# Kernel tuning notes

Hardware: AMD Instinct MI355X
Metric: run time of the kernel (lower is better)

Reference implementation:

```python
import jax, jax.numpy as jnp
import numpy as np

LN_EPS = 1e-5
BN_EPS = 1e-5
HEADS = 8
KERNEL = 31
GROUP_SIZE = 8  # depthwise_conv groups = inner_dim // 8


def _ln(x, g, b):
    mu = jnp.mean(x, axis=-1, keepdims=True)
    var = jnp.var(x, axis=-1, keepdims=True)
    return (x - mu) * jax.lax.rsqrt(var + LN_EPS) * g + b


def _ff(x, g, b, w_in, b_in, w_out, b_out):
    h = _ln(x, g, b)
    y = h @ w_in.T + b_in
    a, c = jnp.split(y, 2, axis=-1)
    return (jax.nn.silu(a) * c) @ w_out.T + b_out


def _attn(x, g, b, wqkv, bqkv, wo, bo):
    B, S, _ = x.shape
    h = _ln(x, g, b)
    qkv = (h @ wqkv.T + bqkv).reshape(B, S, 3, HEADS, -1).transpose(2, 0, 3, 1, 4)
    q, k, v = qkv[0], qkv[1], qkv[2]  # [B,H,S,D]
    scale = q.shape[-1] ** -0.5
    scores = jnp.einsum('bhqd,bhkd->bhqk', q, k) * scale
    w = jax.nn.softmax(scores, axis=-1)
    o = jnp.einsum('bhqk,bhkd->bhqd', w, v)
    o = o.transpose(0, 2, 1, 3).reshape(B, S, -1)
    return o @ wo.T + bo


def _conv(x, g, b, pw1_w, pw1_b, dw_w, dw_b, bn_g, bn_b, bn_m, bn_v, pw2_w, pw2_b):
    h = _ln(x, g, b).transpose(0, 2, 1)  # [B, C, S]
    y = jnp.einsum('oc,bcs->bos', pw1_w[:, :, 0], h) + pw1_b[:, None]
    a, c = jnp.split(y, 2, axis=1)
    y = a * jax.nn.sigmoid(c)  # GLU over channel dim -> [B, inner, S]
    pad = (KERNEL - 1) // 2
    groups = y.shape[1] // dw_w.shape[1]  # inner_dim // 8
    y = jax.lax.conv_general_dilated(
        y, dw_w, window_strides=(1,), padding=[(pad, pad)],
        dimension_numbers=('NCH', 'OIH', 'NCH'), feature_group_count=groups)
    y = y + dw_b[:, None]
    y = (y - bn_m[:, None]) * jax.lax.rsqrt(bn_v[:, None] + BN_EPS) * bn_g[:, None] + bn_b[:, None]
    y = jax.nn.silu(y)
    y = jnp.einsum('oc,bcs->bos', pw2_w[:, :, 0], y) + pw2_b[:, None]
    return y.transpose(0, 2, 1)


def setup_inputs() -> dict:
    key = jax.random.key(0)
    dim, mult, exp = 512, 4, 2
    inner = dim * exp  # 1024
    ks = jax.random.split(key, 16)
    n = lambda k, shp: (jax.random.normal(k, shp, dtype=jnp.float32) * 0.02)
    d = {}
    d['x'] = jax.random.normal(ks[0], (8, 1024, dim), dtype=jnp.float32)
    # ff1
    d['ff1_g'] = jnp.ones((dim,), jnp.float32); d['ff1_b'] = jnp.zeros((dim,), jnp.float32)
    d['ff1_win'] = n(ks[1], (dim * mult * 2, dim)); d['ff1_bin'] = jnp.zeros((dim * mult * 2,), jnp.float32)
    d['ff1_wout'] = n(ks[2], (dim, dim * mult)); d['ff1_bout'] = jnp.zeros((dim,), jnp.float32)
    # attn
    d['attn_g'] = jnp.ones((dim,), jnp.float32); d['attn_b'] = jnp.zeros((dim,), jnp.float32)
    d['wqkv'] = n(ks[3], (3 * dim, dim)); d['bqkv'] = jnp.zeros((3 * dim,), jnp.float32)
    d['wo'] = n(ks[4], (dim, dim)); d['bo'] = jnp.zeros((dim,), jnp.float32)
    # conv
    d['conv_g'] = jnp.ones((dim,), jnp.float32); d['conv_b'] = jnp.zeros((dim,), jnp.float32)
    d['pw1_w'] = n(ks[5], (inner * 2, dim, 1)); d['pw1_b'] = jnp.zeros((inner * 2,), jnp.float32)
    d['dw_w'] = n(ks[6], (inner, GROUP_SIZE, KERNEL)); d['dw_b'] = jnp.zeros((inner,), jnp.float32)
    d['bn_g'] = jnp.ones((inner,), jnp.float32); d['bn_b'] = jnp.zeros((inner,), jnp.float32)
    d['bn_m'] = jnp.zeros((inner,), jnp.float32); d['bn_v'] = jnp.ones((inner,), jnp.float32)
    d['pw2_w'] = n(ks[7], (dim, inner, 1)); d['pw2_b'] = jnp.zeros((dim,), jnp.float32)
    # ff2
    d['ff2_g'] = jnp.ones((dim,), jnp.float32); d['ff2_b'] = jnp.zeros((dim,), jnp.float32)
    d['ff2_win'] = n(ks[8], (dim * mult * 2, dim)); d['ff2_bin'] = jnp.zeros((dim * mult * 2,), jnp.float32)
    d['ff2_wout'] = n(ks[9], (dim, dim * mult)); d['ff2_bout'] = jnp.zeros((dim,), jnp.float32)
    # final norm
    d['fn_g'] = jnp.ones((dim,), jnp.float32); d['fn_b'] = jnp.zeros((dim,), jnp.float32)
    return d


def reference(x, ff1_g, ff1_b, ff1_win, ff1_bin, ff1_wout, ff1_bout,
              attn_g, attn_b, wqkv, bqkv, wo, bo,
              conv_g, conv_b, pw1_w, pw1_b, dw_w, dw_b, bn_g, bn_b, bn_m, bn_v, pw2_w, pw2_b,
              ff2_g, ff2_b, ff2_win, ff2_bin, ff2_wout, ff2_bout, fn_g, fn_b):
    x = x + 0.5 * _ff(x, ff1_g, ff1_b, ff1_win, ff1_bin, ff1_wout, ff1_bout)
    x = x + _attn(x, attn_g, attn_b, wqkv, bqkv, wo, bo)
    x = x + _conv(x, conv_g, conv_b, pw1_w, pw1_b, dw_w, dw_b, bn_g, bn_b, bn_m, bn_v, pw2_w, pw2_b)
    x = x + 0.5 * _ff(x, ff2_g, ff2_b, ff2_win, ff2_bin, ff2_wout, ff2_bout)
    return _ln(x, fn_g, fn_b)
```

## Files before the change

kernel.cpp:

```cpp
#include <hip/hip_runtime.h>

#define SEQ   1024
#define BATCH 8
#define DIM   512
#define NTOK  (SEQ * BATCH)

typedef unsigned short ushort_t;
typedef unsigned int uint_t;
typedef __attribute__((ext_vector_type(8))) short s16x8;
typedef __attribute__((ext_vector_type(4))) float f32x4;

union F4 { float4 v; float f[4]; };

__device__ __forceinline__ float sigmoid_f(float x) { return 1.0f / (1.0f + expf(-x)); }
__device__ __forceinline__ float silu_f(float x)    { return x * sigmoid_f(x); }

__device__ __forceinline__ ushort_t f2bf(float x) {
  uint_t u = __float_as_uint(x);
  return (ushort_t)((u + 0x7FFFu + ((u >> 16) & 1u)) >> 16);
}
__device__ __forceinline__ float bf2f(ushort_t h) {
  return __uint_as_float(((uint_t)h) << 16);
}

__device__ __forceinline__ void gload16(const void* g, void* l) {
  __builtin_amdgcn_global_load_lds(
      (const __attribute__((address_space(1))) void*)g,
      (__attribute__((address_space(3))) void*)l,
      16, 0, 0);
}

struct CastArgs {
  const float* src[8];
  ushort_t*    dst[8];
  int          cum8[8];
};

__global__ __launch_bounds__(256) void f2b_multi(CastArgs a, int total8)
{
  const int i = blockIdx.x * 256 + threadIdx.x;
  if (i >= total8) return;
  int s = 0;
  #pragma unroll
  for (int k = 1; k < 8; ++k) s += (i >= a.cum8[k]) ? 1 : 0;
  const int j = i - a.cum8[s];
  const float* src = a.src[s] + (size_t)j * 8;
  F4 x0, x1;
  x0.v = *(const float4*)(src);
  x1.v = *(const float4*)(src + 4);
  uint4 o;
  o.x = (uint_t)f2bf(x0.f[0]) | ((uint_t)f2bf(x0.f[1]) << 16);
  o.y = (uint_t)f2bf(x0.f[2]) | ((uint_t)f2bf(x0.f[3]) << 16);
  o.z = (uint_t)f2bf(x1.f[0]) | ((uint_t)f2bf(x1.f[1]) << 16);
  o.w = (uint_t)f2bf(x1.f[2]) | ((uint_t)f2bf(x1.f[3]) << 16);
  *(uint4*)(a.dst[s] + (size_t)j * 8) = o;
}

template <int BF>
__global__ __launch_bounds__(256) void ln512_kernel(
    const float* __restrict__ in, const float* __restrict__ g,
    const float* __restrict__ b, void* __restrict__ outv)
{
  const int row = blockIdx.x * 4 + (threadIdx.x >> 6);
  const int l   = threadIdx.x & 63;
  const float* rp = in + (size_t)row * DIM + l * 8;
  F4 v0, v1;
  v0.v = *(const float4*)(rp);
  v1.v = *(const float4*)(rp + 4);
  float sum = 0.f, sq = 0.f;
  #pragma unroll
  for (int j = 0; j < 4; ++j) { sum += v0.f[j] + v1.f[j];
                                sq  += v0.f[j]*v0.f[j] + v1.f[j]*v1.f[j]; }
  #pragma unroll
  for (int m = 32; m >= 1; m >>= 1) {
    sum += __shfl_xor(sum, m, 64);
    sq  += __shfl_xor(sq,  m, 64);
  }
  const float mu   = sum * (1.0f / DIM);
  const float var  = sq * (1.0f / DIM) - mu * mu;
  const float rinv = rsqrtf(var + 1e-5f);
  F4 g0, g1, b0, b1;
  g0.v = *(const float4*)(g + l * 8);     g1.v = *(const float4*)(g + l * 8 + 4);
  b0.v = *(const float4*)(b + l * 8);     b1.v = *(const float4*)(b + l * 8 + 4);
  float o[8];
  #pragma unroll
  for (int j = 0; j < 4; ++j) {
    o[j]     = (v0.f[j] - mu) * rinv * g0.f[j] + b0.f[j];
    o[4 + j] = (v1.f[j] - mu) * rinv * g1.f[j] + b1.f[j];
  }
  if (BF) {
    uint4 u;
    u.x = (uint_t)f2bf(o[0]) | ((uint_t)f2bf(o[1]) << 16);
    u.y = (uint_t)f2bf(o[2]) | ((uint_t)f2bf(o[3]) << 16);
    u.z = (uint_t)f2bf(o[4]) | ((uint_t)f2bf(o[5]) << 16);
    u.w = (uint_t)f2bf(o[6]) | ((uint_t)f2bf(o[7]) << 16);
    *(uint4*)((ushort_t*)outv + (size_t)row * DIM + l * 8) = u;
  } else {
    F4 w0, w1;
    #pragma unroll
    for (int j = 0; j < 4; ++j) { w0.f[j] = o[j]; w1.f[j] = o[4 + j]; }
    *(float4*)((float*)outv + (size_t)row * DIM + l * 8)     = w0.v;
    *(float4*)((float*)outv + (size_t)row * DIM + l * 8 + 4) = w1.v;
  }
}

template <int EPI>
__global__ __launch_bounds__(256) void gemm_bf16(
    const ushort_t* __restrict__ A, const ushort_t* __restrict__ W,
    const float* __restrict__ bias, float* __restrict__ out,
    int N, int K, const float* __restrict__ res, float alpha)
{
  __shared__ ushort_t As[128 * 32];
  __shared__ ushort_t Ws[128 * 32];
  const int t    = threadIdx.x;
  const int lane = t & 63;
  const int w    = t >> 6;
  const int wm   = w >> 1, wn = w & 1;
  const int m0   = blockIdx.y << 7, n0 = blockIdx.x << 7;

  f32x4 acc[4][4] = {};

  const int lds0 = __builtin_amdgcn_readfirstlane((w * 64) * 16);
  const int lds1 = __builtin_amdgcn_readfirstlane((256 + w * 64) * 16);
  const int r0c  = t >> 2;
  const int r1c  = 64 + (t >> 2);
  const int cc   = (t & 3) << 3;

  for (int k0 = 0; k0 < K; k0 += 32) {
    gload16(A + (size_t)(m0 + r0c) * K + k0 + cc, (char*)As + lds0);
    gload16(A + (size_t)(m0 + r1c) * K + k0 + cc, (char*)As + lds1);
    gload16(W + (size_t)(n0 + r0c) * K + k0 + cc, (char*)Ws + lds0);
    gload16(W + (size_t)(n0 + r1c) * K + k0 + cc, (char*)Ws + lds1);
    __syncthreads();
    s16x8 a[4], b[4];
    #pragma unroll
    for (int i = 0; i < 4; ++i)
      a[i] = *(const s16x8*)&As[(wm * 64 + i * 16 + (lane & 15)) * 32 + ((lane >> 4) << 3)];
    #pragma unroll
    for (int j = 0; j < 4; ++j)
      b[j] = *(const s16x8*)&Ws[(wn * 64 + j * 16 + (lane & 15)) * 32 + ((lane >> 4) << 3)];
    #pragma unroll
    for (int i = 0; i < 4; ++i)
      #pragma unroll
      for (int j = 0; j < 4; ++j)
        acc[i][j] = __builtin_amdgcn_mfma_f32_16x16x32_bf16(a[i], b[j], acc[i][j], 0, 0, 0);
    __syncthreads();
  }

  #pragma unroll
  for (int i = 0; i < 4; ++i) {
    #pragma unroll
    for (int j = 0; j < 4; ++j) {
      const int col  = n0 + wn * 64 + j * 16 + (lane & 15);
      const int rowb = m0 + wm * 64 + i * 16 + ((lane >> 4) << 2);
      const float bc = bias[col];
      #pragma unroll
      for (int r = 0; r < 4; ++r) {
        const size_t idx = (size_t)(rowb + r) * N + col;
        float v = acc[i][j][r] + bc;
        if (EPI == 1) v = res[idx] + alpha * v;
        out[idx] = v;
      }
    }
  }
}

__global__ __launch_bounds__(256) void gemm_qkv_bf16(
    const ushort_t* __restrict__ A, const ushort_t* __restrict__ W,
    const float* __restrict__ bias, ushort_t* __restrict__ qkvb,
    ushort_t* __restrict__ Vt, int K)
{
  const int N = 1536;
  __shared__ ushort_t As[128 * 32];
  __shared__ ushort_t Ws[128 * 32];
  const int t    = threadIdx.x;
  const int lane = t & 63;
  const int w    = t >> 6;
  const int wm   = w >> 1, wn = w & 1;
  const int m0   = blockIdx.y << 7, n0 = blockIdx.x << 7;

  f32x4 acc[4][4] = {};

  const int lds0 = __builtin_amdgcn_readfirstlane((w * 64) * 16);
  const int lds1 = __builtin_amdgcn_readfirstlane((256 + w * 64) * 16);
  const int r0c  = t >> 2;
  const int r1c  = 64 + (t >> 2);
  const int cc   = (t & 3) << 3;

  for (int k0 = 0; k0 < K; k0 += 32) {
    gload16(A + (size_t)(m0 + r0c) * K + k0 + cc, (char*)As + lds0);
    gload16(A + (size_t)(m0 + r1c) * K + k0 + cc, (char*)As + lds1);
    gload16(W + (size_t)(n0 + r0c) * K + k0 + cc, (char*)Ws + lds0);
    gload16(W + (size_t)(n0 + r1c) * K + k0 + cc, (char*)Ws + lds1);
    __syncthreads();
    s16x8 a[4], b[4];
    #pragma unroll
    for (int i = 0; i < 4; ++i)
      a[i] = *(const s16x8*)&As[(wm * 64 + i * 16 + (lane & 15)) * 32 + ((lane >> 4) << 3)];
    #pragma unroll
    for (int j = 0; j < 4; ++j)
      b[j] = *(const s16x8*)&Ws[(wn * 64 + j * 16 + (lane & 15)) * 32 + ((lane >> 4) << 3)];
    #pragma unroll
    for (int i = 0; i < 4; ++i)
      #pragma unroll
      for (int j = 0; j < 4; ++j)
        acc[i][j] = __builtin_amdgcn_mfma_f32_16x16x32_bf16(a[i], b[j], acc[i][j], 0, 0, 0);
    __syncthreads();
  }

  #pragma unroll
  for (int i = 0; i < 4; ++i) {
    #pragma unroll
    for (int j = 0; j < 4; ++j) {
      const int col  = n0 + wn * 64 + j * 16 + (lane & 15);
      const int rowb = m0 + wm * 64 + i * 16 + ((lane >> 4) << 2);
      const float bc = bias[col];
      if (col < 1024) {
        #pragma unroll
        for (int r = 0; r < 4; ++r)
          qkvb[(size_t)(rowb + r) * N + col] = f2bf(acc[i][j][r] + bc);
      } else {
        const int vc = col - 1024;
        const int hh = vc >> 6, d = vc & 63;
        const int bb = rowb >> 10, s = rowb & 1023;
        ushort4 o;
        o.x = f2bf(acc[i][j][0] + bc);
        o.y = f2bf(acc[i][j][1] + bc);
        o.z = f2bf(acc[i][j][2] + bc);
        o.w = f2bf(acc[i][j][3] + bc);
        *(ushort4*)&Vt[(size_t)((bb * 8 + hh) * 64 + d) * 1024 + s] = o;
      }
    }
  }
}

template <int CGLU>
__global__ __launch_bounds__(256) void gemm_glu_bf16(
    const ushort_t* __restrict__ A, const ushort_t* __restrict__ W,
    const float* __restrict__ bias, ushort_t* __restrict__ out,
    int NG, int K)
{
  __shared__ ushort_t As[128 * 32];
  __shared__ ushort_t Was[64 * 32];
  __shared__ ushort_t Wcs[64 * 32];
  const int t    = threadIdx.x;
  const int lane = t & 63;
  const int w    = t >> 6;
  const int wm   = w >> 1, wn = w & 1;
  const int m0   = blockIdx.y << 7, n0 = blockIdx.x << 6;

  f32x4 acca[4][2] = {};
  f32x4 accc[4][2] = {};

  const int lds0 = __builtin_amdgcn_readfirstlane((w * 64) * 16);
  const int lds1 = __builtin_amdgcn_readfirstlane((256 + w * 64) * 16);
  const int r0c  = t >> 2;
  const int r1c  = 64 + (t >> 2);
  const int cc   = (t & 3) << 3;

  const ushort_t* Wc = W + (size_t)NG * K;

  for (int k0 = 0; k0 < K; k0 += 32) {
    gload16(A  + (size_t)(m0 + r0c) * K + k0 + cc, (char*)As  + lds0);
    gload16(A  + (size_t)(m0 + r1c) * K + k0 + cc, (char*)As  + lds1);
    gload16(W  + (size_t)(n0 + r0c) * K + k0 + cc, (char*)Was + lds0);
    gload16(Wc + (size_t)(n0 + r0c) * K + k0 + cc, (char*)Wcs + lds0);
    __syncthreads();
    s16x8 a[4], ba[2], bc[2];
    #pragma unroll
    for (int i = 0; i < 4; ++i)
      a[i] = *(const s16x8*)&As[(wm * 64 + i * 16 + (lane & 15)) * 32 + ((lane >> 4) << 3)];
    #pragma unroll
    for (int j = 0; j < 2; ++j) {
      const int roff = (wn * 32 + j * 16 + (lane & 15)) * 32 + ((lane >> 4) << 3);
      ba[j] = *(const s16x8*)&Was[roff];
      bc[j] = *(const s16x8*)&Wcs[roff];
    }
    #pragma unroll
    for (int i = 0; i < 4; ++i)
      #pragma unroll
      for (int j = 0; j < 2; ++j) {
        acca[i][j] = __builtin_amdgcn_mfma_f32_16x16x32_bf16(a[i], ba[j], acca[i][j], 0, 0, 0);
        accc[i][j] = __builtin_amdgcn_mfma_f32_16x16x32_bf16(a[i], bc[j], accc[i][j], 0, 0, 0);
      }
    __syncthreads();
  }

  #pragma unroll
  for (int i = 0; i < 4; ++i) {
    #pragma unroll
    for (int j = 0; j < 2; ++j) {
      const int col  = n0 + wn * 32 + j * 16 + (lane & 15);
      const int rowb = m0 + wm * 64 + i * 16 + ((lane >> 4) << 2);
      const float b1 = bias[col];
      const float b2 = bias[NG + col];
      #pragma unroll
      for (int r = 0; r < 4; ++r) {
        const float av = acca[i][j][r] + b1;
        const float cv = accc[i][j][r] + b2;
        const float o  = CGLU ? (av * sigmoid_f(cv)) : (silu_f(av) * cv);
        out[(size_t)(rowb + r) * NG + col] = f2bf(o);
      }
    }
  }
}

__global__ __launch_bounds__(256) void attn_mfma(
    const ushort_t* __restrict__ qkv, const ushort_t* __restrict__ Vt,
    ushort_t* __restrict__ out)
{
  __shared__ ushort_t Ks[64 * 64];
  __shared__ ushort_t Vs[64 * 64];
  __shared__ ushort_t Ps[4][16 * 64];

  const int t    = threadIdx.x;
  const int lane = t & 63;
  const int w    = t >> 6;
  const int i    = lane & 15;
  const int g    = lane >> 4;
  const int bh   = blockIdx.x;
  const int b    = bh >> 3, h = bh & 7;
  const int qt   = blockIdx.y;

  s16x8 qf[2];
  {
    const ushort_t* qrow = qkv + (size_t)(b * SEQ + qt * 64 + w * 16 + i) * 1536 + h * 64;
    qf[0] = *(const s16x8*)(qrow + g * 8);
    qf[1] = *(const s16x8*)(qrow + 32 + g * 8);
  }

  float m_[4], l_[4];
  f32x4 po[4] = {};
  #pragma unroll
  for (int r = 0; r < 4; ++r) { m_[r] = -1e30f; l_[r] = 0.0f; }

  const int e0   = w * 2;
  const int off0 = __builtin_amdgcn_readfirstlane(e0 * 1024);
  const int off1 = __builtin_amdgcn_readfirstlane(e0 * 1024 + 1024);

  for (int kvt = 0; kvt < 16; ++kvt) {
    __syncthreads();
    {
      const int s_a = e0 * 64 + lane;
      const int ra = s_a >> 3, ca = (s_a & 7) ^ (ra & 7);
      const int s_b = s_a + 64;
      const int rb = s_b >> 3, cb2 = (s_b & 7) ^ (rb & 7);
      gload16(qkv + (size_t)(b * SEQ + kvt * 64 + ra) * 1536 + 512 + h * 64 + ca * 8,
              (char*)Ks + off0);
      gload16(qkv + (size_t)(b * SEQ + kvt * 64 + rb) * 1536 + 512 + h * 64 + cb2 * 8,
              (char*)Ks + off1);
      gload16(Vt + (size_t)(bh * 64 + ra) * SEQ + kvt * 64 + ca * 8,
              (char*)Vs + off0);
      gload16(Vt + (size_t)(bh * 64 + rb) * SEQ + kvt * 64 + cb2 * 8,
              (char*)Vs + off1);
    }
    __syncthreads();

    f32x4 sc[4] = {};
    #pragma unroll
    for (int jj = 0; jj < 4; ++jj) {
      const int row = jj * 16 + i;
      #pragma unroll
      for (int dd = 0; dd < 2; ++dd) {
        const int byteoff = row * 128 + ((dd * 64 + g * 16) ^ ((row & 7) << 4));
        const s16x8 kf = *(const s16x8*)((const char*)Ks + byteoff);
        sc[jj] = __builtin_amdgcn_mfma_f32_16x16x32_bf16(qf[dd], kf, sc[jj], 0, 0, 0);
      }
    }

    #pragma unroll
    for (int r = 0; r < 4; ++r) {
      float v0 = sc[0][r] * 0.125f, v1 = sc[1][r] * 0.125f;
      float v2 = sc[2][r] * 0.125f, v3 = sc[3][r] * 0.125f;
      float mx = fmaxf(fmaxf(v0, v1), fmaxf(v2, v3));
      mx = fmaxf(mx, __shfl_xor(mx, 1));
      mx = fmaxf(mx, __shfl_xor(mx, 2));
      mx = fmaxf(mx, __shfl_xor(mx, 4));
      mx = fmaxf(mx, __shfl_xor(mx, 8));
      const float mn = fmaxf(m_[r], mx);
      const float al = __expf(m_[r] - mn);
      const float p0 = __expf(v0 - mn), p1 = __expf(v1 - mn);
      const float p2 = __expf(v2 - mn), p3 = __expf(v3 - mn);
      float rs = p0 + p1 + p2 + p3;
      rs += __shfl_xor(rs, 1); rs += __shfl_xor(rs, 2);
      rs += __shfl_xor(rs, 4); rs += __shfl_xor(rs, 8);
      l_[r] = l_[r] * al + rs;
      m_[r] = mn;
      #pragma unroll
      for (int dt = 0; dt < 4; ++dt) po[dt][r] *= al;
      const int q = 4 * g + r;
      const int key = (q & 7) << 4;
      ushort_t* pb = &Ps[w][0];
      ((ushort_t*)((char*)pb + q * 128 + ((2 * i) ^ key)))[0]       = f2bf(p0);
      ((ushort_t*)((char*)pb + q * 128 + ((32 + 2 * i) ^ key)))[0]  = f2bf(p1);
      ((ushort_t*)((char*)pb + q * 128 + ((64 + 2 * i) ^ key)))[0]  = f2bf(p2);
      ((ushort_t*)((char*)pb + q * 128 + ((96 + 2 * i) ^ key)))[0]  = f2bf(p3);
    }

    #pragma unroll
    for (int kc = 0; kc < 2; ++kc) {
      const int pbyte = i * 128 + ((kc * 64 + g * 16) ^ ((i & 7) << 4));
      const s16x8 pf = *(const s16x8*)((const char*)&Ps[w][0] + pbyte);
      #pragma unroll
      for (int dt = 0; dt < 4; ++dt) {
        const int vrow = dt * 16 + i;
        const int vbyte = vrow * 128 + ((kc * 64 + g * 16) ^ ((vrow & 7) << 4));
        const s16x8 vf = *(const s16x8*)((const char*)Vs + vbyte);
        po[dt] = __builtin_amdgcn_mfma_f32_16x16x32_bf16(pf, vf, po[dt], 0, 0, 0);
      }
    }
  }

  #pragma unroll
  for (int r = 0; r < 4; ++r) {
    const float inv = 1.0f / l_[r];
    const size_t row = (size_t)(b * SEQ + qt * 64 + w * 16 + 4 * g + r);
    #pragma unroll
    for (int dt = 0; dt < 4; ++dt)
      out[row * 512 + h * 64 + dt * 16 + i] = f2bf(po[dt][r] * inv);
  }
}

__global__ __launch_bounds__(256) void dwconv_kernel(
    const ushort_t* __restrict__ in, const float* __restrict__ w,
    const float* __restrict__ dwb, const float* __restrict__ bng,
    const float* __restrict__ bnb, const float* __restrict__ bnm,
    const float* __restrict__ bnv, ushort_t* __restrict__ out)
{
  __shared__ __align__(16) float tile[94][64];
  const int s0 = blockIdx.x << 6;
  const int c0 = blockIdx.y << 6;
  const int b  = blockIdx.z;
  const int t  = threadIdx.x;

  {
    const int cl4 = (t & 15) << 2;
    #pragma unroll
    for (int it = 0; it < 6; ++it) {
      const int rr = it * 16 + (t >> 4);
      if (rr < 94) {
        const int gs = s0 - 15 + rr;
        float4 fv = make_float4(0.f, 0.f, 0.f, 0.f);
        if (gs >= 0 && gs < SEQ) {
          ushort4 uv = *(const ushort4*)(in + (size_t)(b * SEQ + gs) * 1024 + c0 + cl4);
          fv = make_float4(bf2f(uv.x), bf2f(uv.y), bf2f(uv.z), bf2f(uv.w));
        }
        *(float4*)&tile[rr][cl4] = fv;
      }
    }
  }
  __syncthreads();

  const int c  = t & 63;
  const int sb = (t >> 6) << 4;
  const int gc = c0 + c;

  float acc[16] = {};
  const float* wc = w + (size_t)gc * 248;
  for (int ci = 0; ci < 8; ++ci) {
    const int cl = (c & 56) | ci;
    const float* wp = wc + ci * 31;
    float wt[31];
    #pragma unroll
    for (int a = 0; a < 46; ++a) {
      const float va = tile[sb + a][cl];
      if (a < 31) wt[a] = wp[a];
      #pragma unroll
      for (int j = 0; j < 16; ++j) {
        if (j <= a && a - j <= 30)
          acc[j] = fmaf(wt[a - j], va, acc[j]);
      }
    }
  }

  const float bias = dwb[gc];
  const float mean = bnm[gc];
  const float rstd = rsqrtf(bnv[gc] + 1e-5f);
  const float gg   = bng[gc];
  const float bb2  = bnb[gc];
  #pragma unroll
  for (int j = 0; j < 16; ++j) {
    const int s = s0 + sb + j;
    float y = acc[j] + bias;
    y = (y - mean) * rstd * gg + bb2;
    out[(size_t)(b * SEQ + s) * 1024 + gc] = f2bf(silu_f(y));
  }
}

extern "C" void kernel_launch(void* const* d_in, const int* in_sizes, int n_in,
                              void* d_out, int out_size, void* d_ws, size_t ws_size,
                              hipStream_t stream)
{
  (void)in_sizes; (void)n_in; (void)out_size; (void)ws_size;
  const float* x        = (const float*)d_in[0];
  const float* ff1_g    = (const float*)d_in[1];
  const float* ff1_b    = (const float*)d_in[2];
  const float* ff1_win  = (const float*)d_in[3];
  const float* ff1_bin  = (const float*)d_in[4];
  const float* ff1_wout = (const float*)d_in[5];
  const float* ff1_bout = (const float*)d_in[6];
  const float* attn_g   = (const float*)d_in[7];
  const float* attn_b   = (const float*)d_in[8];
  const float* wqkv     = (const float*)d_in[9];
  const float* bqkv     = (const float*)d_in[10];
  const float* wo       = (const float*)d_in[11];
  const float* bo       = (const float*)d_in[12];
  const float* conv_g   = (const float*)d_in[13];
  const float* conv_b   = (const float*)d_in[14];
  const float* pw1_w    = (const float*)d_in[15];
  const float* pw1_b    = (const float*)d_in[16];
  const float* dw_w     = (const float*)d_in[17];
  const float* dw_b     = (const float*)d_in[18];
  const float* bn_g     = (const float*)d_in[19];
  const float* bn_b     = (const float*)d_in[20];
  const float* bn_m     = (const float*)d_in[21];
  const float* bn_v     = (const float*)d_in[22];
  const float* pw2_w    = (const float*)d_in[23];
  const float* pw2_b    = (const float*)d_in[24];
  const float* ff2_g    = (const float*)d_in[25];
  const float* ff2_b    = (const float*)d_in[26];
  const float* ff2_win  = (const float*)d_in[27];
  const float* ff2_bin  = (const float*)d_in[28];
  const float* ff2_wout = (const float*)d_in[29];
  const float* ff2_bout = (const float*)d_in[30];
  const float* fn_g     = (const float*)d_in[31];
  const float* fn_b     = (const float*)d_in[32];

  char* wsb = (char*)d_ws;
  float*    xc    = (float*)(wsb);
  ushort_t* qkvb  = (ushort_t*)(wsb + (size_t)(16 << 20));
  ushort_t* vtb   = (ushort_t*)(wsb + (size_t)(40 << 20));
  ushort_t* h_bf  = (ushort_t*)(wsb + (size_t)(48 << 20));
  ushort_t* g_bf  = (ushort_t*)(wsb + (size_t)(56 << 20));
  ushort_t* tb_bf = (ushort_t*)(wsb + (size_t)(88 << 20));
  ushort_t* cv_bf = (ushort_t*)(wsb + (size_t)(96 << 20));
  ushort_t* wb    = (ushort_t*)(wsb + (size_t)(112 << 20));

  ushort_t* ff1win_b  = wb;
  ushort_t* ff1wout_b = ff1win_b + 4096 * 512;
  ushort_t* wqkv_b    = ff1wout_b + 512 * 2048;
  ushort_t* wo_b      = wqkv_b + 1536 * 512;
  ushort_t* pw1w_b    = wo_b + 512 * 512;
  ushort_t* pw2w_b    = pw1w_b + 2048 * 512;
  ushort_t* ff2win_b  = pw2w_b + 512 * 1024;
  ushort_t* ff2wout_b = ff2win_b + 4096 * 512;

  float* outp = (float*)d_out;
  const dim3 B256(256);

  {
    CastArgs a;
    const float* srcs[8] = {ff1_win, ff1_wout, wqkv, wo, pw1_w, pw2_w, ff2_win, ff2_wout};
    ushort_t*    dsts[8] = {ff1win_b, ff1wout_b, wqkv_b, wo_b, pw1w_b, pw2w_b, ff2win_b, ff2wout_b};
    const int    ns[8]   = {4096*512, 512*2048, 1536*512, 512*512,
                            2048*512, 512*1024, 4096*512, 512*2048};
    int cum = 0;
    for (int i = 0; i < 8; ++i) {
      a.src[i] = srcs[i]; a.dst[i] = dsts[i]; a.cum8[i] = cum; cum += ns[i] / 8;
    }
    f2b_multi<<<dim3((cum + 255) / 256), B256, 0, stream>>>(a, cum);
  }

  ln512_kernel<1><<<dim3(NTOK / 4), B256, 0, stream>>>(x, ff1_g, ff1_b, h_bf);
  gemm_glu_bf16<0><<<dim3(32, 64), B256, 0, stream>>>(h_bf, ff1win_b, ff1_bin, g_bf, 2048, 512);
  gemm_bf16<1><<<dim3(4, 64), B256, 0, stream>>>(g_bf, ff1wout_b, ff1_bout, xc, 512, 2048, x, 0.5f);

  ln512_kernel<1><<<dim3(NTOK / 4), B256, 0, stream>>>(xc, attn_g, attn_b, h_bf);
  gemm_qkv_bf16<<<dim3(12, 64), B256, 0, stream>>>(h_bf, wqkv_b, bqkv, qkvb, vtb, 512);
  attn_mfma<<<dim3(64, 16), B256, 0, stream>>>(qkvb, vtb, tb_bf);
  gemm_bf16<1><<<dim3(4, 64), B256, 0, stream>>>(tb_bf, wo_b, bo, xc, 512, 512, xc, 1.0f);

  ln512_kernel<1><<<dim3(NTOK / 4), B256, 0, stream>>>(xc, conv_g, conv_b, h_bf);
  gemm_glu_bf16<1><<<dim3(16, 64), B256, 0, stream>>>(h_bf, pw1w_b, pw1_b, g_bf, 1024, 512);
  dwconv_kernel<<<dim3(16, 16, 8), B256, 0, stream>>>(g_bf, dw_w, dw_b, bn_g, bn_b, bn_m, bn_v, cv_bf);
  gemm_bf16<1><<<dim3(4, 64), B256, 0, stream>>>(cv_bf, pw2w_b, pw2_b, xc, 512, 1024, xc, 1.0f);

  ln512_kernel<1><<<dim3(NTOK / 4), B256, 0, stream>>>(xc, ff2_g, ff2_b, h_bf);
  gemm_glu_bf16<0><<<dim3(32, 64), B256, 0, stream>>>(h_bf, ff2win_b, ff2_bin, g_bf, 2048, 512);
  gemm_bf16<1><<<dim3(4, 64), B256, 0, stream>>>(g_bf, ff2wout_b, ff2_bout, xc, 512, 2048, xc, 0.5f);

  ln512_kernel<0><<<dim3(NTOK / 4), B256, 0, stream>>>(xc, fn_g, fn_b, outp);
}
```

Before: 615.9 us.

## Double-buffer LDS tiles in GEMM and attention kernels to overlap loads

```diff
diff --git a/kernel.cpp b/kernel.cpp
--- a/kernel.cpp
+++ b/kernel.cpp
@@ -110,8 +110,8 @@
     const float* __restrict__ bias, float* __restrict__ out,
     int N, int K, const float* __restrict__ res, float alpha)
 {
-  __shared__ ushort_t As[128 * 32];
-  __shared__ ushort_t Ws[128 * 32];
+  __shared__ ushort_t As[2][128 * 32];
+  __shared__ ushort_t Ws[2][128 * 32];
   const int t    = threadIdx.x;
   const int lane = t & 63;
   const int w    = t >> 6;
@@ -126,25 +126,32 @@
   const int r1c  = 64 + (t >> 2);
   const int cc   = (t & 3) << 3;
 
+  auto stage = [&](int buf, int k0) {
+    gload16(A + (size_t)(m0 + r0c) * K + k0 + cc, (char*)As[buf] + lds0);
+    gload16(A + (size_t)(m0 + r1c) * K + k0 + cc, (char*)As[buf] + lds1);
+    gload16(W + (size_t)(n0 + r0c) * K + k0 + cc, (char*)Ws[buf] + lds0);
+    gload16(W + (size_t)(n0 + r1c) * K + k0 + cc, (char*)Ws[buf] + lds1);
+  };
+
+  stage(0, 0);
+  __syncthreads();
+  int cur = 0;
   for (int k0 = 0; k0 < K; k0 += 32) {
-    gload16(A + (size_t)(m0 + r0c) * K + k0 + cc, (char*)As + lds0);
-    gload16(A + (size_t)(m0 + r1c) * K + k0 + cc, (char*)As + lds1);
-    gload16(W + (size_t)(n0 + r0c) * K + k0 + cc, (char*)Ws + lds0);
-    gload16(W + (size_t)(n0 + r1c) * K + k0 + cc, (char*)Ws + lds1);
-    __syncthreads();
+    if (k0 + 32 < K) stage(cur ^ 1, k0 + 32);
     s16x8 a[4], b[4];
     #pragma unroll
     for (int i = 0; i < 4; ++i)
-      a[i] = *(const s16x8*)&As[(wm * 64 + i * 16 + (lane & 15)) * 32 + ((lane >> 4) << 3)];
+      a[i] = *(const s16x8*)&As[cur][(wm * 64 + i * 16 + (lane & 15)) * 32 + ((lane >> 4) << 3)];
     #pragma unroll
     for (int j = 0; j < 4; ++j)
-      b[j] = *(const s16x8*)&Ws[(wn * 64 + j * 16 + (lane & 15)) * 32 + ((lane >> 4) << 3)];
+      b[j] = *(const s16x8*)&Ws[cur][(wn * 64 + j * 16 + (lane & 15)) * 32 + ((lane >> 4) << 3)];
     #pragma unroll
     for (int i = 0; i < 4; ++i)
       #pragma unroll
       for (int j = 0; j < 4; ++j)
         acc[i][j] = __builtin_amdgcn_mfma_f32_16x16x32_bf16(a[i], b[j], acc[i][j], 0, 0, 0);
     __syncthreads();
+    cur ^= 1;
   }
 
   #pragma unroll
@@ -171,8 +178,8 @@
     ushort_t* __restrict__ Vt, int K)
 {
   const int N = 1536;
-  __shared__ ushort_t As[128 * 32];
-  __shared__ ushort_t Ws[128 * 32];
+  __shared__ ushort_t As[2][128 * 32];
+  __shared__ ushort_t Ws[2][128 * 32];
   const int t    = threadIdx.x;
   const int lane = t & 63;
   const int w    = t >> 6;
@@ -187,25 +194,32 @@
   const int r1c  = 64 + (t >> 2);
   const int cc   = (t & 3) << 3;
 
+  auto stage = [&](int buf, int k0) {
+    gload16(A + (size_t)(m0 + r0c) * K + k0 + cc, (char*)As[buf] + lds0);
+    gload16(A + (size_t)(m0 + r1c) * K + k0 + cc, (char*)As[buf] + lds1);
+    gload16(W + (size_t)(n0 + r0c) * K + k0 + cc, (char*)Ws[buf] + lds0);
+    gload16(W + (size_t)(n0 + r1c) * K + k0 + cc, (char*)Ws[buf] + lds1);
+  };
+
+  stage(0, 0);
+  __syncthreads();
+  int cur = 0;
   for (int k0 = 0; k0 < K; k0 += 32) {
-    gload16(A + (size_t)(m0 + r0c) * K + k0 + cc, (char*)As + lds0);
-    gload16(A + (size_t)(m0 + r1c) * K + k0 + cc, (char*)As + lds1);
-    gload16(W + (size_t)(n0 + r0c) * K + k0 + cc, (char*)Ws + lds0);
-    gload16(W + (size_t)(n0 + r1c) * K + k0 + cc, (char*)Ws + lds1);
-    __syncthreads();
+    if (k0 + 32 < K) stage(cur ^ 1, k0 + 32);
     s16x8 a[4], b[4];
     #pragma unroll
     for (int i = 0; i < 4; ++i)
-      a[i] = *(const s16x8*)&As[(wm * 64 + i * 16 + (lane & 15)) * 32 + ((lane >> 4) << 3)];
+      a[i] = *(const s16x8*)&As[cur][(wm * 64 + i * 16 + (lane & 15)) * 32 + ((lane >> 4) << 3)];
     #pragma unroll
     for (int j = 0; j < 4; ++j)
-      b[j] = *(const s16x8*)&Ws[(wn * 64 + j * 16 + (lane & 15)) * 32 + ((lane >> 4) << 3)];
+      b[j] = *(const s16x8*)&Ws[cur][(wn * 64 + j * 16 + (lane & 15)) * 32 + ((lane >> 4) << 3)];
     #pragma unroll
     for (int i = 0; i < 4; ++i)
       #pragma unroll
       for (int j = 0; j < 4; ++j)
         acc[i][j] = __builtin_amdgcn_mfma_f32_16x16x32_bf16(a[i], b[j], acc[i][j], 0, 0, 0);
     __syncthreads();
+    cur ^= 1;
   }
 
   #pragma unroll
@@ -240,9 +254,9 @@
     const float* __restrict__ bias, ushort_t* __restrict__ out,
     int NG, int K)
 {
-  __shared__ ushort_t As[128 * 32];
-  __shared__ ushort_t Was[64 * 32];
-  __shared__ ushort_t Wcs[64 * 32];
+  __shared__ ushort_t As[2][128 * 32];
+  __shared__ ushort_t Was[2][64 * 32];
+  __shared__ ushort_t Wcs[2][64 * 32];
   const int t    = threadIdx.x;
   const int lane = t & 63;
   const int w    = t >> 6;
@@ -260,21 +274,27 @@
 
   const ushort_t* Wc = W + (size_t)NG * K;
 
+  auto stage = [&](int buf, int k0) {
+    gload16(A  + (size_t)(m0 + r0c) * K + k0 + cc, (char*)As[buf]  + lds0);
+    gload16(A  + (size_t)(m0 + r1c) * K + k0 + cc, (char*)As[buf]  + lds1);
+    gload16(W  + (size_t)(n0 + r0c) * K + k0 + cc, (char*)Was[buf] + lds0);
+    gload16(Wc + (size_t)(n0 + r0c) * K + k0 + cc, (char*)Wcs[buf] + lds0);
+  };
+
+  stage(0, 0);
+  __syncthreads();
+  int cur = 0;
   for (int k0 = 0; k0 < K; k0 += 32) {
-    gload16(A  + (size_t)(m0 + r0c) * K + k0 + cc, (char*)As  + lds0);
-    gload16(A  + (size_t)(m0 + r1c) * K + k0 + cc, (char*)As  + lds1);
-    gload16(W  + (size_t)(n0 + r0c) * K + k0 + cc, (char*)Was + lds0);
-    gload16(Wc + (size_t)(n0 + r0c) * K + k0 + cc, (char*)Wcs + lds0);
-    __syncthreads();
+    if (k0 + 32 < K) stage(cur ^ 1, k0 + 32);
     s16x8 a[4], ba[2], bc[2];
     #pragma unroll
     for (int i = 0; i < 4; ++i)
-      a[i] = *(const s16x8*)&As[(wm * 64 + i * 16 + (lane & 15)) * 32 + ((lane >> 4) << 3)];
+      a[i] = *(const s16x8*)&As[cur][(wm * 64 + i * 16 + (lane & 15)) * 32 + ((lane >> 4) << 3)];
     #pragma unroll
     for (int j = 0; j < 2; ++j) {
       const int roff = (wn * 32 + j * 16 + (lane & 15)) * 32 + ((lane >> 4) << 3);
-      ba[j] = *(const s16x8*)&Was[roff];
-      bc[j] = *(const s16x8*)&Wcs[roff];
+      ba[j] = *(const s16x8*)&Was[cur][roff];
+      bc[j] = *(const s16x8*)&Wcs[cur][roff];
     }
     #pragma unroll
     for (int i = 0; i < 4; ++i)
@@ -284,6 +304,7 @@
         accc[i][j] = __builtin_amdgcn_mfma_f32_16x16x32_bf16(a[i], bc[j], accc[i][j], 0, 0, 0);
       }
     __syncthreads();
+    cur ^= 1;
   }
 
   #pragma unroll
@@ -309,8 +330,8 @@
     const ushort_t* __restrict__ qkv, const ushort_t* __restrict__ Vt,
     ushort_t* __restrict__ out)
 {
-  __shared__ ushort_t Ks[64 * 64];
-  __shared__ ushort_t Vs[64 * 64];
+  __shared__ ushort_t Ks[2][64 * 64];
+  __shared__ ushort_t Vs[2][64 * 64];
   __shared__ ushort_t Ps[4][16 * 64];
 
   const int t    = threadIdx.x;
@@ -338,23 +359,27 @@
   const int off0 = __builtin_amdgcn_readfirstlane(e0 * 1024);
   const int off1 = __builtin_amdgcn_readfirstlane(e0 * 1024 + 1024);
 
+  auto stageKV = [&](int buf, int kvt) {
+    const int s_a = e0 * 64 + lane;
+    const int ra = s_a >> 3, ca = (s_a & 7) ^ (ra & 7);
+    const int s_b = s_a + 64;
+    const int rb = s_b >> 3, cb2 = (s_b & 7) ^ (rb & 7);
+    gload16(qkv + (size_t)(b * SEQ + kvt * 64 + ra) * 1536 + 512 + h * 64 + ca * 8,
+            (char*)Ks[buf] + off0);
+    gload16(qkv + (size_t)(b * SEQ + kvt * 64 + rb) * 1536 + 512 + h * 64 + cb2 * 8,
+            (char*)Ks[buf] + off1);
+    gload16(Vt + (size_t)(bh * 64 + ra) * SEQ + kvt * 64 + ca * 8,
+            (char*)Vs[buf] + off0);
+    gload16(Vt + (size_t)(bh * 64 + rb) * SEQ + kvt * 64 + cb2 * 8,
+            (char*)Vs[buf] + off1);
+  };
+
+  stageKV(0, 0);
+  __syncthreads();
+  int cur = 0;
+
   for (int kvt = 0; kvt < 16; ++kvt) {
-    __syncthreads();
-    {
-      const int s_a = e0 * 64 + lane;
-      const int ra = s_a >> 3, ca = (s_a & 7) ^ (ra & 7);
-      const int s_b = s_a + 64;
-      const int rb = s_b >> 3, cb2 = (s_b & 7) ^ (rb & 7);
-      gload16(qkv + (size_t)(b * SEQ + kvt * 64 + ra) * 1536 + 512 + h * 64 + ca * 8,
-              (char*)Ks + off0);
-      gload16(qkv + (size_t)(b * SEQ + kvt * 64 + rb) * 1536 + 512 + h * 64 + cb2 * 8,
-              (char*)Ks + off1);
-      gload16(Vt + (size_t)(bh * 64 + ra) * SEQ + kvt * 64 + ca * 8,
-              (char*)Vs + off0);
-      gload16(Vt + (size_t)(bh * 64 + rb) * SEQ + kvt * 64 + cb2 * 8,
-              (char*)Vs + off1);
-    }
-    __syncthreads();
+    if (kvt + 1 < 16) stageKV(cur ^ 1, kvt + 1);
 
     f32x4 sc[4] = {};
     #pragma unroll
@@ -363,7 +388,7 @@
       #pragma unroll
       for (int dd = 0; dd < 2; ++dd) {
         const int byteoff = row * 128 + ((dd * 64 + g * 16) ^ ((row & 7) << 4));
-        const s16x8 kf = *(const s16x8*)((const char*)Ks + byteoff);
+        const s16x8 kf = *(const s16x8*)((const char*)Ks[cur] + byteoff);
         sc[jj] = __builtin_amdgcn_mfma_f32_16x16x32_bf16(qf[dd], kf, sc[jj], 0, 0, 0);
       }
     }
@@ -405,10 +430,13 @@
       for (int dt = 0; dt < 4; ++dt) {
         const int vrow = dt * 16 + i;
         const int vbyte = vrow * 128 + ((kc * 64 + g * 16) ^ ((vrow & 7) << 4));
-        const s16x8 vf = *(const s16x8*)((const char*)Vs + vbyte);
+        const s16x8 vf = *(const s16x8*)((const char*)Vs[cur] + vbyte);
         po[dt] = __builtin_amdgcn_mfma_f32_16x16x32_bf16(pf, vf, po[dt], 0, 0, 0);
       }
     }
+
+    __syncthreads();
+    cur ^= 1;
   }
 
   #pragma unroll
```

Result: faster. 566.5 us (-8.0%).
